# Kernel optimization log

Hardware: AMD Instinct MI355X
Metric: run time of the kernel (lower is better)

## Reference

```python
import jax, jax.numpy as jnp
import numpy as np

N_BUS = 200000; N_GEN = 50000
E_BB = 1600000; E_GB = 400000; E_BG = 400000
D_IN = 64; H = 32
OUT_BUS = 4; OUT_GEN = 2


def setup_inputs() -> dict:
    key = jax.random.key(0)
    it = iter(jax.random.split(key, 48))
    def nrm(shape, s=0.05):
        return jax.random.normal(next(it), shape, jnp.float32) * s
    inp = {}
    inp["x_bus"] = jax.random.normal(next(it), (N_BUS, D_IN), jnp.float32)
    inp["x_gen"] = jax.random.normal(next(it), (N_GEN, D_IN), jnp.float32)
    inp["src_bb"] = jax.random.randint(next(it), (E_BB,), 0, N_BUS)
    inp["dst_bb"] = jax.random.randint(next(it), (E_BB,), 0, N_BUS)
    inp["src_gb"] = jax.random.randint(next(it), (E_GB,), 0, N_GEN)
    inp["dst_gb"] = jax.random.randint(next(it), (E_GB,), 0, N_BUS)
    inp["src_bg"] = jax.random.randint(next(it), (E_BG,), 0, N_BUS)
    inp["dst_bg"] = jax.random.randint(next(it), (E_BG,), 0, N_GEN)
    # SAGEConv params per layer / relation: lin_l (on aggregated neighbors, with bias),
    # lin_r (root weight on x_dst, no bias) -- matches PyG SAGEConv defaults.
    for lname, din in (("l1", D_IN), ("l2", H)):
        for rel in ("bb", "gb", "bg"):
            inp[f"{lname}_{rel}_Wl"] = nrm((din, H))
            inp[f"{lname}_{rel}_bl"] = jnp.zeros((H,), jnp.float32)
            inp[f"{lname}_{rel}_Wr"] = nrm((din, H))
    for nt, dout in (("bus", OUT_BUS), ("gen", OUT_GEN)):
        inp[f"lin0_{nt}_W"] = nrm((H, H))
        inp[f"lin0_{nt}_b"] = jnp.zeros((H,), jnp.float32)
        inp[f"linf_{nt}_W"] = nrm((H, dout))
        inp[f"linf_{nt}_b"] = jnp.zeros((dout,), jnp.float32)
    return inp


def _sage(x_src, x_dst, src, dst, Wl, bl, Wr, n_dst):
    # SAGEConv: mean-aggregate neighbor features, then out = lin_l(mean) + lin_r(x_dst)
    msg = jax.ops.segment_sum(x_src[src], dst, num_segments=n_dst)
    cnt = jax.ops.segment_sum(jnp.ones((src.shape[0],), x_src.dtype), dst, num_segments=n_dst)
    mean = msg / jnp.maximum(cnt, 1.0)[:, None]
    return mean @ Wl + bl + x_dst @ Wr


def reference(x_bus, x_gen, src_bb, dst_bb, src_gb, dst_gb, src_bg, dst_bg,
              l1_bb_Wl, l1_bb_bl, l1_bb_Wr, l1_gb_Wl, l1_gb_bl, l1_gb_Wr,
              l1_bg_Wl, l1_bg_bl, l1_bg_Wr,
              l2_bb_Wl, l2_bb_bl, l2_bb_Wr, l2_gb_Wl, l2_gb_bl, l2_gb_Wr,
              l2_bg_Wl, l2_bg_bl, l2_bg_Wr,
              lin0_bus_W, lin0_bus_b, lin0_gen_W, lin0_gen_b,
              linf_bus_W, linf_bus_b, linf_gen_W, linf_gen_b):
    # HeteroConv layer 1 (aggr='sum' over relations targeting each dst type)
    hb = (_sage(x_bus, x_bus, src_bb, dst_bb, l1_bb_Wl, l1_bb_bl, l1_bb_Wr, N_BUS)
          + _sage(x_gen, x_bus, src_gb, dst_gb, l1_gb_Wl, l1_gb_bl, l1_gb_Wr, N_BUS))
    hg = _sage(x_bus, x_gen, src_bg, dst_bg, l1_bg_Wl, l1_bg_bl, l1_bg_Wr, N_GEN)
    xb, xg = jax.nn.relu(hb), jax.nn.relu(hg)  # dropout is identity in eval mode
    # HeteroConv layer 2
    hb = (_sage(xb, xb, src_bb, dst_bb, l2_bb_Wl, l2_bb_bl, l2_bb_Wr, N_BUS)
          + _sage(xg, xb, src_gb, dst_gb, l2_gb_Wl, l2_gb_bl, l2_gb_Wr, N_BUS))
    hg = _sage(xb, xg, src_bg, dst_bg, l2_bg_Wl, l2_bg_bl, l2_bg_Wr, N_GEN)
    xb, xg = jax.nn.relu(hb), jax.nn.relu(hg)
    # per-node-type hidden Linear (input relu'd again as in the original; relu is idempotent)
    xb = jax.nn.relu(xb) @ lin0_bus_W + lin0_bus_b
    xg = jax.nn.relu(xg) @ lin0_gen_W + lin0_gen_b
    out_bus = xb @ linf_bus_W + linf_bus_b
    out_gen = xg @ linf_gen_W + linf_gen_b
    return out_bus, out_gen
```

## Files before the change

kernel.cpp:

```cpp
#include <hip/hip_runtime.h>
#include <hip/hip_bf16.h>

#define N_BUS 200000
#define N_GEN 50000
#define E_BB 1600000
#define E_GB 400000
#define E_BG 400000
#define H 32
#define NBINS 1024
#define EPT 16

#define NBK_BUS 782
#define NBK_GEN 196
#define CAP_BB 2560
#define CAP_GB 768
#define CAP_BG 2560

#define NB_PART_BB 391
#define NB_PART_GB 98
#define NB_PART_BG 98
#define NB_PART_ALL 587
#define NB_TF_BUS 782
#define NB_TF_GEN 196
#define NB_PL_BUS 6250
#define NB_PL_GEN 1563

typedef __attribute__((ext_vector_type(8))) short short8;
typedef __attribute__((ext_vector_type(4))) float floatx4;

__device__ inline unsigned short f2bf(float f) {
    __hip_bfloat16 h = __float2bfloat16(f);
    return *reinterpret_cast<unsigned short*>(&h);
}
__device__ inline float bf2f(unsigned short u) {
    return __uint_as_float(((unsigned)u) << 16);
}

__device__ __forceinline__ void part_body(int blk, const int* __restrict__ src,
                                          const int* __restrict__ dst, int nE,
                                          unsigned* __restrict__ cnt_g, int CAP,
                                          unsigned* __restrict__ pairs) {
    __shared__ unsigned hist[NBINS];
    __shared__ unsigned base[NBINS];
    __shared__ unsigned sbase[NBINS];
    __shared__ unsigned sh[256];
    __shared__ unsigned pairv[256 * EPT];
    __shared__ unsigned short bid[256 * EPT];
    const int tid = threadIdx.x;
    const int cbase = blk * (256 * EPT);
    const int total = min(256 * EPT, nE - cbase);

    unsigned es[EPT], ed[EPT];
#pragma unroll
    for (int q = 0; q < EPT; q++) {
        int i = cbase + q * 256 + tid;
        if (i < nE) { es[q] = (unsigned)src[i]; ed[q] = (unsigned)dst[i]; }
        else ed[q] = 0xFFFFFFFFu;
    }
    for (int i = tid; i < NBINS; i += 256) hist[i] = 0;
    __syncthreads();
#pragma unroll
    for (int q = 0; q < EPT; q++)
        if (ed[q] != 0xFFFFFFFFu) atomicAdd(&hist[ed[q] >> 8], 1u);
    __syncthreads();

    unsigned h4[4];
    unsigned s = 0;
#pragma unroll
    for (int k2 = 0; k2 < 4; k2++) { h4[k2] = hist[tid * 4 + k2]; s += h4[k2]; }
    sh[tid] = s;
    __syncthreads();
#pragma unroll
    for (int d = 1; d < 256; d <<= 1) {
        unsigned t = (tid >= d) ? sh[tid - d] : 0u;
        __syncthreads();
        sh[tid] += t;
        __syncthreads();
    }
    unsigned run = sh[tid] - s;
#pragma unroll
    for (int k2 = 0; k2 < 4; k2++) {
        int b = tid * 4 + k2;
        sbase[b] = run;
        base[b] = h4[k2] ? ((unsigned)b * CAP + atomicAdd(&cnt_g[b], h4[k2])) : 0u;
        hist[b] = 0;
        run += h4[k2];
    }
    __syncthreads();

#pragma unroll
    for (int q = 0; q < EPT; q++) {
        if (ed[q] != 0xFFFFFFFFu) {
            unsigned b = ed[q] >> 8;
            unsigned off = atomicAdd(&hist[b], 1u);
            unsigned p = sbase[b] + off;
            pairv[p] = ((ed[q] & 255u) << 24) | es[q];
            bid[p] = (unsigned short)b;
        }
    }
    __syncthreads();

    for (int p = tid; p < total; p += 256) {
        unsigned b = bid[p];
        pairs[base[b] + ((unsigned)p - sbase[b])] = pairv[p];
    }
}

__global__ __launch_bounds__(256) void part_all_kernel(
    const int* __restrict__ sbb, const int* __restrict__ dbb, unsigned* __restrict__ cbb, unsigned* __restrict__ pbb,
    const int* __restrict__ sgb, const int* __restrict__ dgb, unsigned* __restrict__ cgb, unsigned* __restrict__ pgb,
    const int* __restrict__ sbg, const int* __restrict__ dbg, unsigned* __restrict__ cbg, unsigned* __restrict__ pbg)
{
    int b = blockIdx.x;
    if (b < NB_PART_BB) part_body(b, sbb, dbb, E_BB, cbb, CAP_BB, pbb);
    else if (b < NB_PART_BB + NB_PART_GB) part_body(b - NB_PART_BB, sgb, dgb, E_GB, cgb, CAP_GB, pgb);
    else part_body(b - NB_PART_BB - NB_PART_GB, sbg, dbg, E_BG, cbg, CAP_BG, pbg);
}

__device__ __forceinline__ void fine_body(int b, const unsigned* __restrict__ cnt_g, int CAP,
                                          const unsigned* __restrict__ pairs,
                                          unsigned* __restrict__ rs,
                                          unsigned* __restrict__ esrc, int nDst) {
    __shared__ unsigned cnt[256];
    __shared__ unsigned sh[256];
    __shared__ unsigned stg[2560];
    const int tid = threadIdx.x;
    const unsigned start = (unsigned)b * CAP;
    const unsigned m = cnt_g[b];
    const unsigned end = start + m;

    cnt[tid] = 0;
    __syncthreads();
    for (unsigned k = start + tid; k < end; k += 256)
        atomicAdd(&cnt[pairs[k] >> 24], 1u);
    __syncthreads();
    unsigned c = cnt[tid];
    sh[tid] = c;
    __syncthreads();
#pragma unroll
    for (int d = 1; d < 256; d <<= 1) {
        unsigned t = (tid >= d) ? sh[tid - d] : 0u;
        __syncthreads();
        sh[tid] += t;
        __syncthreads();
    }
    int gd = b * 256 + tid;
    unsigned rowstart = start + sh[tid] - c;
    if (gd < nDst) rs[gd] = (rowstart << 9) | (c < 511u ? c : 511u);
    cnt[tid] = sh[tid] - c;
    __syncthreads();
    for (unsigned k = start + tid; k < end; k += 256) {
        unsigned p = pairs[k];
        unsigned off = atomicAdd(&cnt[p >> 24], 1u);
        stg[off] = p & 0x00FFFFFFu;
    }
    __syncthreads();
    for (unsigned p = tid; p < m; p += 256) esrc[start + p] = stg[p];
}

__global__ __launch_bounds__(256) void fine_all_kernel(
    const unsigned* __restrict__ cbb, const unsigned* __restrict__ pbb, unsigned* __restrict__ rsbb, unsigned* __restrict__ ebb,
    const unsigned* __restrict__ cgb, const unsigned* __restrict__ pgb, unsigned* __restrict__ rsgb, unsigned* __restrict__ egb,
    const unsigned* __restrict__ cbg, const unsigned* __restrict__ pbg, unsigned* __restrict__ rsbg, unsigned* __restrict__ ebg)
{
    int b = blockIdx.x;
    if (b < NBK_BUS) fine_body(b, cbb, CAP_BB, pbb, rsbb, ebb, N_BUS);
    else if (b < 2 * NBK_BUS) fine_body(b - NBK_BUS, cgb, CAP_GB, pgb, rsgb, egb, N_BUS);
    else fine_body(b - 2 * NBK_BUS, cbg, CAP_BG, pbg, rsbg, ebg, N_GEN);
}

__global__ __launch_bounds__(256) void prep_kernel(
    const float* __restrict__ l1_bb_Wl, const float* __restrict__ l1_bb_bl, const float* __restrict__ l1_bb_Wr,
    const float* __restrict__ l1_gb_Wl, const float* __restrict__ l1_gb_bl, const float* __restrict__ l1_gb_Wr,
    const float* __restrict__ l1_bg_Wl, const float* __restrict__ l1_bg_bl, const float* __restrict__ l1_bg_Wr,
    const float* __restrict__ l2_bb_Wl, const float* __restrict__ l2_bb_bl, const float* __restrict__ l2_bb_Wr,
    const float* __restrict__ l2_gb_Wl, const float* __restrict__ l2_gb_bl, const float* __restrict__ l2_gb_Wr,
    const float* __restrict__ l2_bg_Wl, const float* __restrict__ l2_bg_bl, const float* __restrict__ l2_bg_Wr,
    const float* __restrict__ lin0_bus_W, const float* __restrict__ lin0_bus_b,
    const float* __restrict__ linf_bus_W, const float* __restrict__ linf_bus_b,
    const float* __restrict__ lin0_gen_W, const float* __restrict__ lin0_gen_b,
    const float* __restrict__ linf_gen_W, const float* __restrict__ linf_gen_b,
    unsigned short* __restrict__ Wf1b, float* __restrict__ B1b,
    unsigned short* __restrict__ Wf1g, float* __restrict__ B1g,
    unsigned short* __restrict__ Wf2b, float* __restrict__ B2b,
    unsigned short* __restrict__ Wf2g, float* __restrict__ B2g,
    float* __restrict__ WeB, float* __restrict__ beB,
    float* __restrict__ WeG, float* __restrict__ beG,
    unsigned* __restrict__ cursors)
{
    int t0 = blockIdx.x * 256 + threadIdx.x;
    int NT = gridDim.x * 256;

    if (t0 < 3 * NBINS) cursors[t0] = 0u;

    for (int f = t0; f < 2 * 6 * 64 * 8; f += NT) {
        int j = f & 7, l = (f >> 3) & 63, tile = f >> 9;
        int nt = tile % 6, kt = tile / 6;
        int k = kt * 32 + (l >> 4) * 8 + j, n = nt * 16 + (l & 15);
        float v;
        if (n < 32) v = l1_bb_Wl[k * 32 + n];
        else if (n < 64) v = l1_bg_Wl[k * 32 + n - 32];
        else v = l1_bb_Wr[k * 32 + n - 64] + l1_gb_Wr[k * 32 + n - 64];
        Wf1b[f] = f2bf(v);
    }
    for (int f = t0; f < 2 * 4 * 64 * 8; f += NT) {
        int j = f & 7, l = (f >> 3) & 63, tile = f >> 9;
        int nt = tile % 4, kt = tile / 4;
        int k = kt * 32 + (l >> 4) * 8 + j, n = nt * 16 + (l & 15);
        float v = (n < 32) ? l1_gb_Wl[k * 32 + n] : l1_bg_Wr[k * 32 + n - 32];
        Wf1g[f] = f2bf(v);
    }
    for (int f = t0; f < 6 * 64 * 8; f += NT) {
        int j = f & 7, l = (f >> 3) & 63, nt = f >> 9;
        int k = (l >> 4) * 8 + j, n = nt * 16 + (l & 15);
        float v;
        if (n < 32) v = l2_bb_Wl[k * 32 + n];
        else if (n < 64) v = l2_bg_Wl[k * 32 + n - 32];
        else v = l2_bb_Wr[k * 32 + n - 64] + l2_gb_Wr[k * 32 + n - 64];
        Wf2b[f] = f2bf(v);
    }
    for (int f = t0; f < 4 * 64 * 8; f += NT) {
        int j = f & 7, l = (f >> 3) & 63, nt = f >> 9;
        int k = (l >> 4) * 8 + j, n = nt * 16 + (l & 15);
        float v = (n < 32) ? l2_gb_Wl[k * 32 + n] : l2_bg_Wr[k * 32 + n - 32];
        Wf2g[f] = f2bf(v);
    }
    if (t0 < 96) {
        B1b[t0] = (t0 < 64) ? 0.0f : l1_bb_bl[t0 - 64] + l1_gb_bl[t0 - 64];
        B2b[t0] = (t0 < 64) ? 0.0f : l2_bb_bl[t0 - 64] + l2_gb_bl[t0 - 64];
    }
    if (t0 < 64) {
        B1g[t0] = (t0 < 32) ? 0.0f : l1_bg_bl[t0 - 32];
        B2g[t0] = (t0 < 32) ? 0.0f : l2_bg_bl[t0 - 32];
    }
    if (t0 < 128) {
        int k = t0 >> 2, c = t0 & 3;
        float s = 0.0f;
        for (int m = 0; m < 32; m++) s += lin0_bus_W[k * 32 + m] * linf_bus_W[m * 4 + c];
        WeB[t0] = s;
    }
    if (t0 >= 128 && t0 < 132) {
        int c = t0 - 128;
        float s = linf_bus_b[c];
        for (int m = 0; m < 32; m++) s += lin0_bus_b[m] * linf_bus_W[m * 4 + c];
        beB[c] = s;
    }
    if (t0 >= 132 && t0 < 196) {
        int i = t0 - 132, k = i >> 1, c = i & 1;
        float s = 0.0f;
        for (int m = 0; m < 32; m++) s += lin0_gen_W[k * 32 + m] * linf_gen_W[m * 2 + c];
        WeG[i] = s;
    }
    if (t0 >= 196 && t0 < 198) {
        int c = t0 - 196;
        float s = linf_gen_b[c];
        for (int m = 0; m < 32; m++) s += lin0_gen_b[m] * linf_gen_W[m * 2 + c];
        beG[c] = s;
    }
}

template <int K, int NOUT>
__device__ __forceinline__ void mfma_tail(
    int rows, int base,
    const unsigned short* __restrict__ Wf, const float* __restrict__ bias,
    unsigned short* __restrict__ y0, unsigned short* __restrict__ y1, float* __restrict__ h,
    char* ldsraw)
{
    constexpr int KT = K / 32, NTN = NOUT / 16, NCH = NOUT / 32;
    constexpr int XS = K + 8;
    constexpr int OS = 34;
    short* lx = (short*)ldsraw;
    float* lo = (float*)ldsraw;
    const int tid = threadIdx.x;
    const int w = tid >> 6, l = tid & 63, quad = l >> 4, ln = l & 15;

    short8 bf[KT][NTN];
    const short8* wf8 = (const short8*)Wf;
#pragma unroll
    for (int kt = 0; kt < KT; kt++)
#pragma unroll
        for (int nt = 0; nt < NTN; nt++)
            bf[kt][nt] = wf8[(kt * NTN + nt) * 64 + l];
    float bv[NTN];
#pragma unroll
    for (int nt = 0; nt < NTN; nt++) bv[nt] = bias[nt * 16 + ln];

    floatx4 acc[4][NTN];
#pragma unroll
    for (int mt = 0; mt < 4; mt++)
#pragma unroll
        for (int nt = 0; nt < NTN; nt++) {
            floatx4 c0 = {bv[nt], bv[nt], bv[nt], bv[nt]};
            acc[mt][nt] = c0;
        }
#pragma unroll
    for (int mt = 0; mt < 4; mt++) {
        const int row = w * 64 + mt * 16 + ln;
#pragma unroll
        for (int kt = 0; kt < KT; kt++) {
            short8 af = *(const short8*)&lx[row * XS + kt * 32 + quad * 8];
#pragma unroll
            for (int nt = 0; nt < NTN; nt++)
                acc[mt][nt] = __builtin_amdgcn_mfma_f32_16x16x32_bf16(
                    af, bf[kt][nt], acc[mt][nt], 0, 0, 0);
        }
    }

#pragma unroll
    for (int c = 0; c < NCH; c++) {
        __syncthreads();
#pragma unroll
        for (int mt = 0; mt < 4; mt++)
#pragma unroll
            for (int d = 0; d < 2; d++) {
                int nt = 2 * c + d;
#pragma unroll
                for (int r = 0; r < 4; r++)
                    lo[(w * 64 + mt * 16 + quad * 4 + r) * OS + d * 16 + ln] = acc[mt][nt][r];
            }
        __syncthreads();
        const int T4 = rows * 8;
        if (c == NCH - 1) {
            float* og = h + (size_t)base * 32;
            for (int q = tid; q < T4; q += 256) {
                int r = q >> 3, cc = (q & 7) * 4;
                const float* p = &lo[r * OS + cc];
                *(float4*)(og + q * 4) = make_float4(p[0], p[1], p[2], p[3]);
            }
        } else {
            unsigned short* og = ((c == 0) ? y0 : y1) + (size_t)base * 32;
            for (int q = tid; q < T4; q += 256) {
                int r = q >> 3, cc = (q & 7) * 4;
                const float* p = &lo[r * OS + cc];
                short4 s4;
                s4.x = (short)f2bf(p[0]); s4.y = (short)f2bf(p[1]);
                s4.z = (short)f2bf(p[2]); s4.w = (short)f2bf(p[3]);
                *(short4*)(og + q * 4) = s4;
            }
        }
    }
}

template <int K, int NOUT>
__device__ __forceinline__ void transform_body(
    int blk, const float* x, int n,
    const unsigned short* __restrict__ Wf, const float* __restrict__ bias,
    unsigned short* __restrict__ y0, unsigned short* __restrict__ y1, float* h,
    char* ldsraw)
{
    constexpr int XS = K + 8;
    short* lx = (short*)ldsraw;
    const int tid = threadIdx.x;
    const int base = blk * 256;
    const int rows = min(256, n - base);

    {
        const float4* xg = (const float4*)(x + (size_t)base * K);
        const int T4 = rows * (K / 4);
        for (int q = tid; q < T4; q += 256) {
            float4 v = xg[q];
            int r = q / (K / 4), c = (q % (K / 4)) * 4;
            short4 s4;
            s4.x = (short)f2bf(v.x); s4.y = (short)f2bf(v.y);
            s4.z = (short)f2bf(v.z); s4.w = (short)f2bf(v.w);
            *(short4*)&lx[r * XS + c] = s4;
        }
    }
    __syncthreads();
    mfma_tail<K, NOUT>(rows, base, Wf, bias, y0, y1, h, ldsraw);
}

template <int NOUT>
__device__ __forceinline__ void transform_bf16_body(
    int blk, const unsigned short* x, int n,
    const unsigned short* __restrict__ Wf, const float* __restrict__ bias,
    unsigned short* __restrict__ y0, unsigned short* __restrict__ y1, float* h,
    char* ldsraw)
{
    constexpr int K = 32, XS = K + 8;
    short* lx = (short*)ldsraw;
    const int tid = threadIdx.x;
    const int base = blk * 256;
    const int rows = min(256, n - base);

    {
        const short8* xg = (const short8*)(x + (size_t)base * K);
        const int T8 = rows * (K / 8);
        for (int q = tid; q < T8; q += 256) {
            short8 v = xg[q];
            int r = q / (K / 8), c = (q % (K / 8)) * 8;
            *(short8*)&lx[r * XS + c] = v;
        }
    }
    __syncthreads();
    mfma_tail<K, NOUT>(rows, base, Wf, bias, y0, y1, h, ldsraw);
}

__global__ __launch_bounds__(256) void tf1_all_kernel(
    const float* xb, const unsigned short* __restrict__ Wfb, const float* __restrict__ Bb,
    unsigned short* __restrict__ yb0, unsigned short* __restrict__ yb1, float* hb,
    const float* xg, const unsigned short* __restrict__ Wfg, const float* __restrict__ Bg,
    unsigned short* __restrict__ yg0, float* hg)
{
    constexpr int XB = 256 * (64 + 8) * 2, OB = 256 * 34 * 4;
    __shared__ __align__(16) char ldsraw[(XB > OB) ? XB : OB];
    int b = blockIdx.x;
    if (b < NB_TF_BUS)
        transform_body<64, 96>(b, xb, N_BUS, Wfb, Bb, yb0, yb1, hb, ldsraw);
    else
        transform_body<64, 64>(b - NB_TF_BUS, xg, N_GEN, Wfg, Bg, yg0, nullptr, hg, ldsraw);
}

__global__ __launch_bounds__(256) void tf2b_all_kernel(
    const unsigned short* x2b, const unsigned short* __restrict__ Wfb, const float* __restrict__ Bb,
    unsigned short* __restrict__ yb0, unsigned short* __restrict__ yb1, float* hb,
    const unsigned short* x2g, const unsigned short* __restrict__ Wfg, const float* __restrict__ Bg,
    unsigned short* __restrict__ yg0, float* hg)
{
    constexpr int XB = 256 * (32 + 8) * 2, OB = 256 * 34 * 4;
    __shared__ __align__(16) char ldsraw[(XB > OB) ? XB : OB];
    int b = blockIdx.x;
    if (b < NB_TF_BUS)
        transform_bf16_body<96>(b, x2b, N_BUS, Wfb, Bb, yb0, yb1, hb, ldsraw);
    else
        transform_bf16_body<64>(b - NB_TF_BUS, x2g, N_GEN, Wfg, Bg, yg0, nullptr, hg, ldsraw);
}

__device__ __forceinline__ void agg_one(
    unsigned u, const unsigned* __restrict__ e,
    const unsigned short* __restrict__ y, int j, float4& r)
{
    unsigned k0 = u >> 9;
    unsigned c = u & 511u;
    unsigned k1 = k0 + c;
    float4 a0 = make_float4(0.f, 0.f, 0.f, 0.f);
    float4 a1 = a0, a2 = a0, a3 = a0;
    unsigned k = k0;
    if (k + 4 <= k1) {
        unsigned s0 = e[k], s1 = e[k + 1], s2 = e[k + 2], s3 = e[k + 3];
        for (; k + 8 <= k1; k += 4) {
            unsigned t0 = e[k + 4], t1 = e[k + 5], t2 = e[k + 6], t3 = e[k + 7];
            ushort4 v0 = *(const ushort4*)(y + (size_t)s0 * H + j);
            ushort4 v1 = *(const ushort4*)(y + (size_t)s1 * H + j);
            ushort4 v2 = *(const ushort4*)(y + (size_t)s2 * H + j);
            ushort4 v3 = *(const ushort4*)(y + (size_t)s3 * H + j);
            a0.x += bf2f(v0.x); a0.y += bf2f(v0.y); a0.z += bf2f(v0.z); a0.w += bf2f(v0.w);
            a1.x += bf2f(v1.x); a1.y += bf2f(v1.y); a1.z += bf2f(v1.z); a1.w += bf2f(v1.w);
            a2.x += bf2f(v2.x); a2.y += bf2f(v2.y); a2.z += bf2f(v2.z); a2.w += bf2f(v2.w);
            a3.x += bf2f(v3.x); a3.y += bf2f(v3.y); a3.z += bf2f(v3.z); a3.w += bf2f(v3.w);
            s0 = t0; s1 = t1; s2 = t2; s3 = t3;
        }
        {
            ushort4 v0 = *(const ushort4*)(y + (size_t)s0 * H + j);
            ushort4 v1 = *(const ushort4*)(y + (size_t)s1 * H + j);
            ushort4 v2 = *(const ushort4*)(y + (size_t)s2 * H + j);
            ushort4 v3 = *(const ushort4*)(y + (size_t)s3 * H + j);
            a0.x += bf2f(v0.x); a0.y += bf2f(v0.y); a0.z += bf2f(v0.z); a0.w += bf2f(v0.w);
            a1.x += bf2f(v1.x); a1.y += bf2f(v1.y); a1.z += bf2f(v1.z); a1.w += bf2f(v1.w);
            a2.x += bf2f(v2.x); a2.y += bf2f(v2.y); a2.z += bf2f(v2.z); a2.w += bf2f(v2.w);
            a3.x += bf2f(v3.x); a3.y += bf2f(v3.y); a3.z += bf2f(v3.z); a3.w += bf2f(v3.w);
            k += 4;
        }
    }
    for (; k < k1; ++k) {
        unsigned s = e[k];
        const ushort4 v = *(const ushort4*)(y + (size_t)s * H + j);
        a0.x += bf2f(v.x); a0.y += bf2f(v.y); a0.z += bf2f(v.z); a0.w += bf2f(v.w);
    }
    a0.x += a1.x + a2.x + a3.x; a0.y += a1.y + a2.y + a3.y;
    a0.z += a1.z + a2.z + a3.z; a0.w += a1.w + a2.w + a3.w;
    float inv = 1.0f / (float)(c > 1u ? c : 1u);
    r.x += a0.x * inv; r.y += a0.y * inv; r.z += a0.z * inv; r.w += a0.w * inv;
}

template <bool FUSE>
__device__ __forceinline__ void pull_body(
    int blk, bool hasB, int n,
    const unsigned* __restrict__ rsA, const unsigned* __restrict__ eA, const unsigned short* __restrict__ yA,
    const unsigned* __restrict__ rsB, const unsigned* __restrict__ eB, const unsigned short* __restrict__ yB,
    const float* __restrict__ h, unsigned short* __restrict__ x2,
    const float* __restrict__ We, const float* __restrict__ be, int DOUT, float* __restrict__ outp)
{
    const int tid = threadIdx.x;
    unsigned node = blk * 32u + (tid >> 3);
    int j = (tid & 7) * 4;
    if (node >= (unsigned)n) return;

    float4 r = *(const float4*)(h + (size_t)node * H + j);

    agg_one(rsA[node], eA, yA, j, r);
    if (hasB) agg_one(rsB[node], eB, yB, j, r);

    if (!FUSE) {
        ushort4 o;
        o.x = f2bf(fmaxf(r.x, 0.f)); o.y = f2bf(fmaxf(r.y, 0.f));
        o.z = f2bf(fmaxf(r.z, 0.f)); o.w = f2bf(fmaxf(r.w, 0.f));
        *(ushort4*)(x2 + (size_t)node * H + j) = o;
        return;
    }

    float p0 = fmaxf(r.x, 0.f), p1 = fmaxf(r.y, 0.f), p2 = fmaxf(r.z, 0.f), p3 = fmaxf(r.w, 0.f);
    float tot[4];
#pragma unroll
    for (int c = 0; c < 4; c++) {
        if (c < DOUT) {
            tot[c] = p0 * We[(j + 0) * DOUT + c] + p1 * We[(j + 1) * DOUT + c]
                   + p2 * We[(j + 2) * DOUT + c] + p3 * We[(j + 3) * DOUT + c];
        } else tot[c] = 0.f;
    }
#pragma unroll
    for (int mask = 1; mask <= 4; mask <<= 1) {
#pragma unroll
        for (int c = 0; c < 4; c++) tot[c] += __shfl_xor(tot[c], mask);
    }
    if ((tid & 7) == 0) {
        if (DOUT == 4) {
            *(float4*)(outp + (size_t)node * 4) =
                make_float4(tot[0] + be[0], tot[1] + be[1], tot[2] + be[2], tot[3] + be[3]);
        } else {
            *(float2*)(outp + (size_t)node * 2) = make_float2(tot[0] + be[0], tot[1] + be[1]);
        }
    }
}

template <bool FUSE>
__global__ __launch_bounds__(256) void pull_all_kernel(
    const unsigned* __restrict__ rsbb, const unsigned* __restrict__ ebb, const unsigned short* __restrict__ ybb,
    const unsigned* __restrict__ rsgb, const unsigned* __restrict__ egb, const unsigned short* __restrict__ ygb,
    const float* __restrict__ hb, unsigned short* __restrict__ x2b,
    const float* __restrict__ WeB, const float* __restrict__ beB,
    const unsigned* __restrict__ rsbg, const unsigned* __restrict__ ebg, const unsigned short* __restrict__ ybg,
    const float* __restrict__ hg, unsigned short* __restrict__ x2g,
    const float* __restrict__ WeG, const float* __restrict__ beG,
    float* __restrict__ outp)
{
    int b = blockIdx.x;
    if (b < NB_PL_BUS)
        pull_body<FUSE>(b, true, N_BUS, rsbb, ebb, ybb, rsgb, egb, ygb, hb, x2b, WeB, beB, 4, outp);
    else
        pull_body<FUSE>(b - NB_PL_BUS, false, N_GEN, rsbg, ebg, ybg, nullptr, nullptr, nullptr,
                        hg, x2g, WeG, beG, 2, outp ? outp + (size_t)N_BUS * 4 : nullptr);
}

extern "C" void kernel_launch(void* const* d_in, const int* in_sizes, int n_in,
                              void* d_out, int out_size, void* d_ws, size_t ws_size,
                              hipStream_t stream) {
    const float* x_bus = (const float*)d_in[0];
    const float* x_gen = (const float*)d_in[1];
    const int* src_bb = (const int*)d_in[2];
    const int* dst_bb = (const int*)d_in[3];
    const int* src_gb = (const int*)d_in[4];
    const int* dst_gb = (const int*)d_in[5];
    const int* src_bg = (const int*)d_in[6];
    const int* dst_bg = (const int*)d_in[7];
    const float* l1_bb_Wl = (const float*)d_in[8];
    const float* l1_bb_bl = (const float*)d_in[9];
    const float* l1_bb_Wr = (const float*)d_in[10];
    const float* l1_gb_Wl = (const float*)d_in[11];
    const float* l1_gb_bl = (const float*)d_in[12];
    const float* l1_gb_Wr = (const float*)d_in[13];
    const float* l1_bg_Wl = (const float*)d_in[14];
    const float* l1_bg_bl = (const float*)d_in[15];
    const float* l1_bg_Wr = (const float*)d_in[16];
    const float* l2_bb_Wl = (const float*)d_in[17];
    const float* l2_bb_bl = (const float*)d_in[18];
    const float* l2_bb_Wr = (const float*)d_in[19];
    const float* l2_gb_Wl = (const float*)d_in[20];
    const float* l2_gb_bl = (const float*)d_in[21];
    const float* l2_gb_Wr = (const float*)d_in[22];
    const float* l2_bg_Wl = (const float*)d_in[23];
    const float* l2_bg_bl = (const float*)d_in[24];
    const float* l2_bg_Wr = (const float*)d_in[25];
    const float* lin0_bus_W = (const float*)d_in[26];
    const float* lin0_bus_b = (const float*)d_in[27];
    const float* linf_bus_W = (const float*)d_in[28];
    const float* linf_bus_b = (const float*)d_in[29];
    const float* lin0_gen_W = (const float*)d_in[30];
    const float* lin0_gen_b = (const float*)d_in[31];
    const float* linf_gen_W = (const float*)d_in[32];
    const float* linf_gen_b = (const float*)d_in[33];

    char* ws = (char*)d_ws;
    size_t off = 0;
    auto alloc = [&](size_t bytes) {
        char* p = ws + off;
        off += (bytes + 255) & ~(size_t)255;
        return p;
    };
    unsigned* rs_bb = (unsigned*)alloc((size_t)N_BUS * 4);
    unsigned* rs_gb = (unsigned*)alloc((size_t)N_BUS * 4);
    unsigned* rs_bg = (unsigned*)alloc((size_t)N_GEN * 4);
    unsigned* cur_bb = (unsigned*)alloc(NBINS * 4);
    unsigned* cur_gb = (unsigned*)alloc(NBINS * 4);
    unsigned* cur_bg = (unsigned*)alloc(NBINS * 4);
    unsigned* e_bb = (unsigned*)alloc((size_t)NBK_BUS * CAP_BB * 4);
    unsigned* e_gb = (unsigned*)alloc((size_t)NBK_BUS * CAP_GB * 4);
    unsigned* e_bg = (unsigned*)alloc((size_t)NBK_GEN * CAP_BG * 4);
    unsigned* p_bb = (unsigned*)alloc((size_t)NBK_BUS * CAP_BB * 4);
    unsigned* p_gb = (unsigned*)alloc((size_t)NBK_BUS * CAP_GB * 4);
    unsigned* p_bg = (unsigned*)alloc((size_t)NBK_GEN * CAP_BG * 4);
    unsigned short* y_bb = (unsigned short*)alloc((size_t)N_BUS * H * 2);
    unsigned short* y_bg = (unsigned short*)alloc((size_t)N_BUS * H * 2);
    unsigned short* y_gb = (unsigned short*)alloc((size_t)N_GEN * H * 2);
    float* h_bus = (float*)alloc((size_t)N_BUS * H * 4);
    float* h_gen = (float*)alloc((size_t)N_GEN * H * 4);
    unsigned short* x2_bus = (unsigned short*)alloc((size_t)N_BUS * H * 2);
    unsigned short* x2_gen = (unsigned short*)alloc((size_t)N_GEN * H * 2);
    unsigned short* Wf1b = (unsigned short*)alloc(2 * 6 * 64 * 8 * 2);
    float* B1b = (float*)alloc(96 * 4);
    unsigned short* Wf1g = (unsigned short*)alloc(2 * 4 * 64 * 8 * 2);
    float* B1g = (float*)alloc(64 * 4);
    unsigned short* Wf2b = (unsigned short*)alloc(6 * 64 * 8 * 2);
    float* B2b = (float*)alloc(96 * 4);
    unsigned short* Wf2g = (unsigned short*)alloc(4 * 64 * 8 * 2);
    float* B2g = (float*)alloc(64 * 4);
    float* WeB = (float*)alloc(128 * 4);
    float* beB = (float*)alloc(4 * 4);
    float* WeG = (float*)alloc(64 * 4);
    float* beG = (float*)alloc(2 * 4);

    prep_kernel<<<32, 256, 0, stream>>>(
        l1_bb_Wl, l1_bb_bl, l1_bb_Wr, l1_gb_Wl, l1_gb_bl, l1_gb_Wr,
        l1_bg_Wl, l1_bg_bl, l1_bg_Wr, l2_bb_Wl, l2_bb_bl, l2_bb_Wr,
        l2_gb_Wl, l2_gb_bl, l2_gb_Wr, l2_bg_Wl, l2_bg_bl, l2_bg_Wr,
        lin0_bus_W, lin0_bus_b, linf_bus_W, linf_bus_b,
        lin0_gen_W, lin0_gen_b, linf_gen_W, linf_gen_b,
        Wf1b, B1b, Wf1g, B1g, Wf2b, B2b, Wf2g, B2g, WeB, beB, WeG, beG,
        cur_bb);

    part_all_kernel<<<NB_PART_ALL, 256, 0, stream>>>(
        src_bb, dst_bb, cur_bb, p_bb, src_gb, dst_gb, cur_gb, p_gb, src_bg, dst_bg, cur_bg, p_bg);

    fine_all_kernel<<<2 * NBK_BUS + NBK_GEN, 256, 0, stream>>>(
        cur_bb, p_bb, rs_bb, e_bb, cur_gb, p_gb, rs_gb, e_gb, cur_bg, p_bg, rs_bg, e_bg);

    tf1_all_kernel<<<NB_TF_BUS + NB_TF_GEN, 256, 0, stream>>>(
        x_bus, Wf1b, B1b, y_bb, y_bg, h_bus, x_gen, Wf1g, B1g, y_gb, h_gen);

    pull_all_kernel<false><<<NB_PL_BUS + NB_PL_GEN, 256, 0, stream>>>(
        rs_bb, e_bb, y_bb, rs_gb, e_gb, y_gb, h_bus, x2_bus, WeB, beB,
        rs_bg, e_bg, y_bg, h_gen, x2_gen, WeG, beG, nullptr);

    tf2b_all_kernel<<<NB_TF_BUS + NB_TF_GEN, 256, 0, stream>>>(
        x2_bus, Wf2b, B2b, y_bb, y_bg, h_bus, x2_gen, Wf2g, B2g, y_gb, h_gen);

    pull_all_kernel<true><<<NB_PL_BUS + NB_PL_GEN, 256, 0, stream>>>(
        rs_bb, e_bb, y_bb, rs_gb, e_gb, y_gb, h_bus, nullptr, WeB, beB,
        rs_bg, e_bg, y_bg, h_gen, nullptr, WeG, beG, (float*)d_out);
}
```

Measured before the change: 351.7 us.

## Merge weight prep into partition launch and fine sort into layer-1 transform

Splits cursor zeroing into a tiny standalone kernel. Weight packing now runs as extra blocks of the coarse partition kernel, and the fine per-bucket sort runs as extra blocks of the layer-1 transform kernel, sharing its LDS buffer. This cuts the launch count from six to five and lets independent work overlap inside one grid, removing the tail-drain bubbles between small kernels. The fused fine blocks now take the transform kernel's larger LDS allocation, which may reduce their occupancy.

```diff
diff --git a/kernel.cpp b/kernel.cpp
--- a/kernel.cpp
+++ b/kernel.cpp
@@ -20,10 +20,15 @@
 #define NB_PART_GB 98
 #define NB_PART_BG 98
 #define NB_PART_ALL 587
+#define NB_PREP 32
 #define NB_TF_BUS 782
 #define NB_TF_GEN 196
+#define NB_TF_ALL 978
+#define NB_FINE_ALL 1760
 #define NB_PL_BUS 6250
 #define NB_PL_GEN 1563
+
+#define PNONE 0xFFFFFFFFu
 
 typedef __attribute__((ext_vector_type(8))) short short8;
 typedef __attribute__((ext_vector_type(4))) float floatx4;
@@ -34,6 +39,11 @@
 }
 __device__ inline float bf2f(unsigned short u) {
     return __uint_as_float(((unsigned)u) << 16);
+}
+
+__global__ __launch_bounds__(256) void zero_kernel(unsigned* __restrict__ p) {
+    int i = blockIdx.x * 256 + threadIdx.x;
+    if (i < 3 * NBINS) p[i] = 0u;
 }
 
 __device__ __forceinline__ void part_body(int blk, const int* __restrict__ src,
@@ -55,13 +65,13 @@
     for (int q = 0; q < EPT; q++) {
         int i = cbase + q * 256 + tid;
         if (i < nE) { es[q] = (unsigned)src[i]; ed[q] = (unsigned)dst[i]; }
-        else ed[q] = 0xFFFFFFFFu;
+        else ed[q] = PNONE;
     }
     for (int i = tid; i < NBINS; i += 256) hist[i] = 0;
     __syncthreads();
 #pragma unroll
     for (int q = 0; q < EPT; q++)
-        if (ed[q] != 0xFFFFFFFFu) atomicAdd(&hist[ed[q] >> 8], 1u);
+        if (ed[q] != PNONE) atomicAdd(&hist[ed[q] >> 8], 1u);
     __syncthreads();
 
     unsigned h4[4];
@@ -90,7 +100,7 @@
 
 #pragma unroll
     for (int q = 0; q < EPT; q++) {
-        if (ed[q] != 0xFFFFFFFFu) {
+        if (ed[q] != PNONE) {
             unsigned b = ed[q] >> 8;
             unsigned off = atomicAdd(&hist[b], 1u);
             unsigned p = sbase[b] + off;
@@ -106,70 +116,7 @@
     }
 }
 
-__global__ __launch_bounds__(256) void part_all_kernel(
-    const int* __restrict__ sbb, const int* __restrict__ dbb, unsigned* __restrict__ cbb, unsigned* __restrict__ pbb,
-    const int* __restrict__ sgb, const int* __restrict__ dgb, unsigned* __restrict__ cgb, unsigned* __restrict__ pgb,
-    const int* __restrict__ sbg, const int* __restrict__ dbg, unsigned* __restrict__ cbg, unsigned* __restrict__ pbg)
-{
-    int b = blockIdx.x;
-    if (b < NB_PART_BB) part_body(b, sbb, dbb, E_BB, cbb, CAP_BB, pbb);
-    else if (b < NB_PART_BB + NB_PART_GB) part_body(b - NB_PART_BB, sgb, dgb, E_GB, cgb, CAP_GB, pgb);
-    else part_body(b - NB_PART_BB - NB_PART_GB, sbg, dbg, E_BG, cbg, CAP_BG, pbg);
-}
-
-__device__ __forceinline__ void fine_body(int b, const unsigned* __restrict__ cnt_g, int CAP,
-                                          const unsigned* __restrict__ pairs,
-                                          unsigned* __restrict__ rs,
-                                          unsigned* __restrict__ esrc, int nDst) {
-    __shared__ unsigned cnt[256];
-    __shared__ unsigned sh[256];
-    __shared__ unsigned stg[2560];
-    const int tid = threadIdx.x;
-    const unsigned start = (unsigned)b * CAP;
-    const unsigned m = cnt_g[b];
-    const unsigned end = start + m;
-
-    cnt[tid] = 0;
-    __syncthreads();
-    for (unsigned k = start + tid; k < end; k += 256)
-        atomicAdd(&cnt[pairs[k] >> 24], 1u);
-    __syncthreads();
-    unsigned c = cnt[tid];
-    sh[tid] = c;
-    __syncthreads();
-#pragma unroll
-    for (int d = 1; d < 256; d <<= 1) {
-        unsigned t = (tid >= d) ? sh[tid - d] : 0u;
-        __syncthreads();
-        sh[tid] += t;
-        __syncthreads();
-    }
-    int gd = b * 256 + tid;
-    unsigned rowstart = start + sh[tid] - c;
-    if (gd < nDst) rs[gd] = (rowstart << 9) | (c < 511u ? c : 511u);
-    cnt[tid] = sh[tid] - c;
-    __syncthreads();
-    for (unsigned k = start + tid; k < end; k += 256) {
-        unsigned p = pairs[k];
-        unsigned off = atomicAdd(&cnt[p >> 24], 1u);
-        stg[off] = p & 0x00FFFFFFu;
-    }
-    __syncthreads();
-    for (unsigned p = tid; p < m; p += 256) esrc[start + p] = stg[p];
-}
-
-__global__ __launch_bounds__(256) void fine_all_kernel(
-    const unsigned* __restrict__ cbb, const unsigned* __restrict__ pbb, unsigned* __restrict__ rsbb, unsigned* __restrict__ ebb,
-    const unsigned* __restrict__ cgb, const unsigned* __restrict__ pgb, unsigned* __restrict__ rsgb, unsigned* __restrict__ egb,
-    const unsigned* __restrict__ cbg, const unsigned* __restrict__ pbg, unsigned* __restrict__ rsbg, unsigned* __restrict__ ebg)
-{
-    int b = blockIdx.x;
-    if (b < NBK_BUS) fine_body(b, cbb, CAP_BB, pbb, rsbb, ebb, N_BUS);
-    else if (b < 2 * NBK_BUS) fine_body(b - NBK_BUS, cgb, CAP_GB, pgb, rsgb, egb, N_BUS);
-    else fine_body(b - 2 * NBK_BUS, cbg, CAP_BG, pbg, rsbg, ebg, N_GEN);
-}
-
-__global__ __launch_bounds__(256) void prep_kernel(
+__device__ __forceinline__ void prep_body(int pb,
     const float* __restrict__ l1_bb_Wl, const float* __restrict__ l1_bb_bl, const float* __restrict__ l1_bb_Wr,
     const float* __restrict__ l1_gb_Wl, const float* __restrict__ l1_gb_bl, const float* __restrict__ l1_gb_Wr,
     const float* __restrict__ l1_bg_Wl, const float* __restrict__ l1_bg_bl, const float* __restrict__ l1_bg_Wr,
@@ -185,13 +132,10 @@
     unsigned short* __restrict__ Wf2b, float* __restrict__ B2b,
     unsigned short* __restrict__ Wf2g, float* __restrict__ B2g,
     float* __restrict__ WeB, float* __restrict__ beB,
-    float* __restrict__ WeG, float* __restrict__ beG,
-    unsigned* __restrict__ cursors)
-{
-    int t0 = blockIdx.x * 256 + threadIdx.x;
-    int NT = gridDim.x * 256;
-
-    if (t0 < 3 * NBINS) cursors[t0] = 0u;
+    float* __restrict__ WeG, float* __restrict__ beG)
+{
+    int t0 = pb * 256 + threadIdx.x;
+    const int NT = NB_PREP * 256;
 
     for (int f = t0; f < 2 * 6 * 64 * 8; f += NT) {
         int j = f & 7, l = (f >> 3) & 63, tile = f >> 9;
@@ -259,18 +203,91 @@
     }
 }
 
-template <int K, int NOUT>
+__global__ __launch_bounds__(256) void prep_part_kernel(
+    const int* __restrict__ sbb, const int* __restrict__ dbb, unsigned* __restrict__ cbb, unsigned* __restrict__ pbb,
+    const int* __restrict__ sgb, const int* __restrict__ dgb, unsigned* __restrict__ cgb, unsigned* __restrict__ pgb,
+    const int* __restrict__ sbg, const int* __restrict__ dbg, unsigned* __restrict__ cbg, unsigned* __restrict__ pbg,
+    const float* __restrict__ l1_bb_Wl, const float* __restrict__ l1_bb_bl, const float* __restrict__ l1_bb_Wr,
+    const float* __restrict__ l1_gb_Wl, const float* __restrict__ l1_gb_bl, const float* __restrict__ l1_gb_Wr,
+    const float* __restrict__ l1_bg_Wl, const float* __restrict__ l1_bg_bl, const float* __restrict__ l1_bg_Wr,
+    const float* __restrict__ l2_bb_Wl, const float* __restrict__ l2_bb_bl, const float* __restrict__ l2_bb_Wr,
+    const float* __restrict__ l2_gb_Wl, const float* __restrict__ l2_gb_bl, const float* __restrict__ l2_gb_Wr,
+    const float* __restrict__ l2_bg_Wl, const float* __restrict__ l2_bg_bl, const float* __restrict__ l2_bg_Wr,
+    const float* __restrict__ lin0_bus_W, const float* __restrict__ lin0_bus_b,
+    const float* __restrict__ linf_bus_W, const float* __restrict__ linf_bus_b,
+    const float* __restrict__ lin0_gen_W, const float* __restrict__ lin0_gen_b,
+    const float* __restrict__ linf_gen_W, const float* __restrict__ linf_gen_b,
+    unsigned short* __restrict__ Wf1b, float* __restrict__ B1b,
+    unsigned short* __restrict__ Wf1g, float* __restrict__ B1g,
+    unsigned short* __restrict__ Wf2b, float* __restrict__ B2b,
+    unsigned short* __restrict__ Wf2g, float* __restrict__ B2g,
+    float* __restrict__ WeB, float* __restrict__ beB,
+    float* __restrict__ WeG, float* __restrict__ beG)
+{
+    int b = blockIdx.x;
+    if (b < NB_PART_BB) part_body(b, sbb, dbb, E_BB, cbb, CAP_BB, pbb);
+    else if (b < NB_PART_BB + NB_PART_GB) part_body(b - NB_PART_BB, sgb, dgb, E_GB, cgb, CAP_GB, pgb);
+    else if (b < NB_PART_ALL) part_body(b - NB_PART_BB - NB_PART_GB, sbg, dbg, E_BG, cbg, CAP_BG, pbg);
+    else prep_body(b - NB_PART_ALL,
+                   l1_bb_Wl, l1_bb_bl, l1_bb_Wr, l1_gb_Wl, l1_gb_bl, l1_gb_Wr,
+                   l1_bg_Wl, l1_bg_bl, l1_bg_Wr, l2_bb_Wl, l2_bb_bl, l2_bb_Wr,
+                   l2_gb_Wl, l2_gb_bl, l2_gb_Wr, l2_bg_Wl, l2_bg_bl, l2_bg_Wr,
+                   lin0_bus_W, lin0_bus_b, linf_bus_W, linf_bus_b,
+                   lin0_gen_W, lin0_gen_b, linf_gen_W, linf_gen_b,
+                   Wf1b, B1b, Wf1g, B1g, Wf2b, B2b, Wf2g, B2g, WeB, beB, WeG, beG);
+}
+
+__device__ __forceinline__ void fine_body(int b, const unsigned* __restrict__ cnt_g, int CAP,
+                                          const unsigned* __restrict__ pairs,
+                                          unsigned* __restrict__ rs,
+                                          unsigned* __restrict__ esrc, int nDst,
+                                          char* __restrict__ lds) {
+    unsigned* cnt = (unsigned*)lds;
+    unsigned* sh = (unsigned*)(lds + 1024);
+    unsigned* stg = (unsigned*)(lds + 2048);
+    const int tid = threadIdx.x;
+    const unsigned start = (unsigned)b * CAP;
+    const unsigned m = cnt_g[b];
+    const unsigned end = start + m;
+
+    cnt[tid] = 0;
+    __syncthreads();
+    for (unsigned k = start + tid; k < end; k += 256)
+        atomicAdd(&cnt[pairs[k] >> 24], 1u);
+    __syncthreads();
+    unsigned c = cnt[tid];
+    sh[tid] = c;
+    __syncthreads();
+#pragma unroll
+    for (int d = 1; d < 256; d <<= 1) {
+        unsigned t = (tid >= d) ? sh[tid - d] : 0u;
+        __syncthreads();
+        sh[tid] += t;
+        __syncthreads();
+    }
+    int gd = b * 256 + tid;
+    unsigned rowstart = start + sh[tid] - c;
+    if (gd < nDst) rs[gd] = (rowstart << 9) | (c < 511u ? c : 511u);
+    cnt[tid] = sh[tid] - c;
+    __syncthreads();
+    for (unsigned k = start + tid; k < end; k += 256) {
+        unsigned p = pairs[k];
+        unsigned off = atomicAdd(&cnt[p >> 24], 1u);
+        stg[off] = p & 0x00FFFFFFu;
+    }
+    __syncthreads();
+    for (unsigned p = tid; p < m; p += 256) esrc[start + p] = stg[p];
+}
+
+template <int K, int NOUT, int XS>
 __device__ __forceinline__ void mfma_tail(
     int rows, int base,
     const unsigned short* __restrict__ Wf, const float* __restrict__ bias,
     unsigned short* __restrict__ y0, unsigned short* __restrict__ y1, float* __restrict__ h,
-    char* ldsraw)
+    short* lx, float* lo)
 {
     constexpr int KT = K / 32, NTN = NOUT / 16, NCH = NOUT / 32;
-    constexpr int XS = K + 8;
     constexpr int OS = 34;
-    short* lx = (short*)ldsraw;
-    float* lo = (float*)ldsraw;
     const int tid = threadIdx.x;
     const int w = tid >> 6, l = tid & 63, quad = l >> 4, ln = l & 15;
 
@@ -367,7 +384,7 @@
         }
     }
     __syncthreads();
-    mfma_tail<K, NOUT>(rows, base, Wf, bias, y0, y1, h, ldsraw);
+    mfma_tail<K, NOUT, XS>(rows, base, Wf, bias, y0, y1, h, (short*)ldsraw, (float*)ldsraw);
 }
 
 template <int NOUT>
@@ -393,22 +410,31 @@
         }
     }
     __syncthreads();
-    mfma_tail<K, NOUT>(rows, base, Wf, bias, y0, y1, h, ldsraw);
-}
-
-__global__ __launch_bounds__(256) void tf1_all_kernel(
+    mfma_tail<32, NOUT, XS>(rows, base, Wf, bias, y0, y1, h, (short*)ldsraw, (float*)ldsraw);
+}
+
+__global__ __launch_bounds__(256) void tf1_fine_kernel(
     const float* xb, const unsigned short* __restrict__ Wfb, const float* __restrict__ Bb,
     unsigned short* __restrict__ yb0, unsigned short* __restrict__ yb1, float* hb,
     const float* xg, const unsigned short* __restrict__ Wfg, const float* __restrict__ Bg,
-    unsigned short* __restrict__ yg0, float* hg)
+    unsigned short* __restrict__ yg0, float* hg,
+    const unsigned* __restrict__ cbb, const unsigned* __restrict__ pbb, unsigned* __restrict__ rsbb, unsigned* __restrict__ ebb,
+    const unsigned* __restrict__ cgb, const unsigned* __restrict__ pgb, unsigned* __restrict__ rsgb, unsigned* __restrict__ egb,
+    const unsigned* __restrict__ cbg, const unsigned* __restrict__ pbg, unsigned* __restrict__ rsbg, unsigned* __restrict__ ebg)
 {
     constexpr int XB = 256 * (64 + 8) * 2, OB = 256 * 34 * 4;
     __shared__ __align__(16) char ldsraw[(XB > OB) ? XB : OB];
     int b = blockIdx.x;
     if (b < NB_TF_BUS)
         transform_body<64, 96>(b, xb, N_BUS, Wfb, Bb, yb0, yb1, hb, ldsraw);
-    else
+    else if (b < NB_TF_ALL)
         transform_body<64, 64>(b - NB_TF_BUS, xg, N_GEN, Wfg, Bg, yg0, nullptr, hg, ldsraw);
+    else {
+        int f = b - NB_TF_ALL;
+        if (f < NBK_BUS) fine_body(f, cbb, CAP_BB, pbb, rsbb, ebb, N_BUS, ldsraw);
+        else if (f < 2 * NBK_BUS) fine_body(f - NBK_BUS, cgb, CAP_GB, pgb, rsgb, egb, N_BUS, ldsraw);
+        else fine_body(f - 2 * NBK_BUS, cbg, CAP_BG, pbg, rsbg, ebg, N_GEN, ldsraw);
+    }
 }
 
 __global__ __launch_bounds__(256) void tf2b_all_kernel(
@@ -619,23 +645,21 @@
     float* WeG = (float*)alloc(64 * 4);
     float* beG = (float*)alloc(2 * 4);
 
-    prep_kernel<<<32, 256, 0, stream>>>(
+    zero_kernel<<<12, 256, 0, stream>>>(cur_bb);
+
+    prep_part_kernel<<<NB_PART_ALL + NB_PREP, 256, 0, stream>>>(
+        src_bb, dst_bb, cur_bb, p_bb, src_gb, dst_gb, cur_gb, p_gb,
+        src_bg, dst_bg, cur_bg, p_bg,
         l1_bb_Wl, l1_bb_bl, l1_bb_Wr, l1_gb_Wl, l1_gb_bl, l1_gb_Wr,
         l1_bg_Wl, l1_bg_bl, l1_bg_Wr, l2_bb_Wl, l2_bb_bl, l2_bb_Wr,
         l2_gb_Wl, l2_gb_bl, l2_gb_Wr, l2_bg_Wl, l2_bg_bl, l2_bg_Wr,
         lin0_bus_W, lin0_bus_b, linf_bus_W, linf_bus_b,
         lin0_gen_W, lin0_gen_b, linf_gen_W, linf_gen_b,
-        Wf1b, B1b, Wf1g, B1g, Wf2b, B2b, Wf2g, B2g, WeB, beB, WeG, beG,
-        cur_bb);
-
-    part_all_kernel<<<NB_PART_ALL, 256, 0, stream>>>(
-        src_bb, dst_bb, cur_bb, p_bb, src_gb, dst_gb, cur_gb, p_gb, src_bg, dst_bg, cur_bg, p_bg);
-
-    fine_all_kernel<<<2 * NBK_BUS + NBK_GEN, 256, 0, stream>>>(
+        Wf1b, B1b, Wf1g, B1g, Wf2b, B2b, Wf2g, B2g, WeB, beB, WeG, beG);
+
+    tf1_fine_kernel<<<NB_TF_ALL + NB_FINE_ALL, 256, 0, stream>>>(
+        x_bus, Wf1b, B1b, y_bb, y_bg, h_bus, x_gen, Wf1g, B1g, y_gb, h_gen,
         cur_bb, p_bb, rs_bb, e_bb, cur_gb, p_gb, rs_gb, e_gb, cur_bg, p_bg, rs_bg, e_bg);
-
-    tf1_all_kernel<<<NB_TF_BUS + NB_TF_GEN, 256, 0, stream>>>(
-        x_bus, Wf1b, B1b, y_bb, y_bg, h_bus, x_gen, Wf1g, B1g, y_gb, h_gen);
 
     pull_all_kernel<false><<<NB_PL_BUS + NB_PL_GEN, 256, 0, stream>>>(
         rs_bb, e_bb, y_bb, rs_gb, e_gb, y_gb, h_bus, x2_bus, WeB, beB,
```

Measured after the change: 354.3 us. No clear change (+0.7%).
